# Performance work log

Hardware: AMD Instinct MI355X
Metric: run time of the kernel (lower is better)

## Reference

```python
import jax, jax.numpy as jnp
import numpy as np

DIM = 1024
N_HEADS = 16
HEAD_DIM = DIM // N_HEADS  # 64
THETA = 10000.0
B, S = 4, 1024


def _rope_full_dim(x):
    """RoPE applied over the FULL last dim (head_dim == model dim), matching the
    original module which builds RotaryEmbeddings(head_dim=args.dim) and applies
    it to [B, S, dim] before splitting into heads. Positions start at 0."""
    Bx, Sx, D = x.shape
    freq = 1.0 / (THETA ** (jnp.arange(0, D, 2, dtype=jnp.float32) / D))  # [D/2]
    ang = jnp.arange(Sx, dtype=jnp.float32)[:, None] * freq[None, :]      # [S, D/2]
    cos, sin = jnp.cos(ang), jnp.sin(ang)
    xp = x.astype(jnp.float32).reshape(Bx, Sx, D // 2, 2)
    x0, x1 = xp[..., 0], xp[..., 1]
    rot = jnp.stack([x0 * cos - x1 * sin, x0 * sin + x1 * cos], axis=-1)
    return rot.reshape(Bx, Sx, D).astype(x.dtype)


def setup_inputs() -> dict:
    key = jax.random.key(0)
    ks = jax.random.split(key, 5)
    scale = 1.0 / np.sqrt(DIM)
    x = jax.random.normal(ks[0], (B, S, DIM), dtype=jnp.float32)
    Wq = jax.random.normal(ks[1], (DIM, DIM), dtype=jnp.float32) * scale
    Wk = jax.random.normal(ks[2], (DIM, DIM), dtype=jnp.float32) * scale
    Wv = jax.random.normal(ks[3], (DIM, DIM), dtype=jnp.float32) * scale
    Wo = jax.random.normal(ks[4], (DIM, DIM), dtype=jnp.float32) * scale
    bo = jnp.zeros((DIM,), dtype=jnp.float32)
    return {"x": x, "Wq": Wq, "Wk": Wk, "Wv": Wv, "Wo": Wo, "bo": bo, "start_pos": 0}


def reference(x, Wq, Wk, Wv, Wo, bo, start_pos):
    # start_pos == 0: the zero-initialized KV cache write+read is an identity
    # (keys == xk, values == xv over [:, :S]); n_rep == 1 so repeat_kv is a no-op.
    # NOTE: the original applies NO causal mask.
    Bx, Sx, _ = x.shape
    xq = _rope_full_dim(x @ Wq.T)  # [B, S, DIM] (weights stored torch-style [out,in])
    xk = _rope_full_dim(x @ Wk.T)
    xv = x @ Wv.T
    q = xq.reshape(Bx, Sx, N_HEADS, HEAD_DIM).transpose(0, 2, 1, 3)  # [B,H,S,D]
    k = xk.reshape(Bx, Sx, N_HEADS, HEAD_DIM).transpose(0, 2, 1, 3)
    v = xv.reshape(Bx, Sx, N_HEADS, HEAD_DIM).transpose(0, 2, 1, 3)
    scores = jnp.einsum("bhqd,bhkd->bhqk", q, k) / np.float32(np.sqrt(HEAD_DIM))
    attn = jax.nn.softmax(scores.astype(jnp.float32), axis=-1).astype(q.dtype)
    out = jnp.einsum("bhqk,bhkd->bhqd", attn, v)          # [B,H,S,D]
    out = out.transpose(0, 2, 1, 3).reshape(Bx, Sx, DIM)  # [B,S,DIM]
    return out @ Wo.T + bo
```

## Files before the change

kernel.cpp:

```cpp
#include <hip/hip_runtime.h>
#include <cstdint>
#include <cstddef>

typedef _Float16 f16;
typedef __attribute__((ext_vector_type(8))) _Float16 h8v;
typedef __attribute__((ext_vector_type(4))) _Float16 h4v;
typedef __attribute__((ext_vector_type(4))) float f4v;

#define DIM 1024
#define SEQ 1024
#define NH 16
#define HD 64

__device__ __forceinline__ void gld16(const void* g, void* l) {
  __builtin_amdgcn_global_load_lds(
      (const __attribute__((address_space(1))) void*)g,
      (__attribute__((address_space(3))) void*)l, 16, 0, 0);
}

__device__ __forceinline__ f4v mfma16(h8v a, h8v b, f4v c) {
  return __builtin_amdgcn_mfma_f32_16x16x32_f16(a, b, c, 0, 0, 0);
}
__device__ __forceinline__ f4v mfma16k16(h4v a, h4v b, f4v c) {
  return __builtin_amdgcn_mfma_f32_16x16x16f16(a, b, c, 0, 0, 0);
}

__device__ __forceinline__ void cvt_store4(f16* dst, float4 v) {
  *(h4v*)dst = (h4v){(f16)v.x, (f16)v.y, (f16)v.z, (f16)v.w};
}

__global__ __launch_bounds__(256) void convert_kernel(
    const float* __restrict__ x,  const float* __restrict__ Wq,
    const float* __restrict__ Wk, const float* __restrict__ Wv,
    const float* __restrict__ Wo,
    f16* __restrict__ xh, f16* __restrict__ wqkv, f16* __restrict__ woh)
{
  int i = blockIdx.x * 256 + threadIdx.x;
  cvt_store4(xh + 4 * (size_t)i, ((const float4*)x)[i]);
  if (i < DIM * DIM / 4) {
    cvt_store4(wqkv + 4 * (size_t)i,               ((const float4*)Wq)[i]);
    cvt_store4(wqkv + DIM * DIM + 4 * (size_t)i,   ((const float4*)Wk)[i]);
    cvt_store4(wqkv + 2 * DIM * DIM + 4 * (size_t)i, ((const float4*)Wv)[i]);
    cvt_store4(woh + 4 * (size_t)i,                ((const float4*)Wo)[i]);
  }
}

__global__ __launch_bounds__(256) void qkv_gemm(
    const f16* __restrict__ A, const f16* __restrict__ W,
    f16* __restrict__ Qh, f16* __restrict__ Kh, f16* __restrict__ Vt)
{
  __shared__ f16 lA[128 * 32];
  __shared__ f16 lB[128 * 32];
  const int m0 = blockIdx.x * 128;
  const int n0 = blockIdx.y * 128;
  const int tid = threadIdx.x;
  const int w = tid >> 6, lane = tid & 63, quad = lane >> 4, l16 = lane & 15;
  const int wm = (w >> 1) * 64, wn = (w & 1) * 64;

  const int c0 = tid, c1 = 256 + tid;
  const int r0 = c0 >> 2, kc0 = (c0 & 3) ^ ((r0 >> 1) & 3);
  const int r1 = c1 >> 2, kc1 = (c1 & 3) ^ ((r1 >> 1) & 3);
  const f16* gA0 = A + (size_t)(m0 + r0) * DIM + kc0 * 8;
  const f16* gA1 = A + (size_t)(m0 + r1) * DIM + kc1 * 8;
  const f16* gB0 = W + (size_t)(n0 + r0) * DIM + kc0 * 8;
  const f16* gB1 = W + (size_t)(n0 + r1) * DIM + kc1 * 8;
  f16* lA0 = &lA[(c0 & ~63) * 8];
  f16* lA1 = &lA[(c1 & ~63) * 8];
  f16* lB0 = &lB[(c0 & ~63) * 8];
  f16* lB1 = &lB[(c1 & ~63) * 8];

  int pA[4], pB[4];
#pragma unroll
  for (int t = 0; t < 4; ++t) {
    int r = wm + t * 16 + l16;
    pA[t] = r * 4 + (quad ^ ((r >> 1) & 3));
    int rn = wn + t * 16 + l16;
    pB[t] = rn * 4 + (quad ^ ((rn >> 1) & 3));
  }

  f4v acc[4][4] = {};
  for (int kt = 0; kt < DIM / 32; ++kt) {
    const int ko = kt * 32;
    gld16(gA0 + ko, lA0);
    gld16(gA1 + ko, lA1);
    gld16(gB0 + ko, lB0);
    gld16(gB1 + ko, lB1);
    __syncthreads();
    h8v af[4], bf[4];
#pragma unroll
    for (int t = 0; t < 4; ++t) af[t] = *(const h8v*)&lA[pA[t] * 8];
#pragma unroll
    for (int t = 0; t < 4; ++t) bf[t] = *(const h8v*)&lB[pB[t] * 8];
#pragma unroll
    for (int i = 0; i < 4; ++i)
#pragma unroll
      for (int j = 0; j < 4; ++j)
        acc[i][j] = mfma16(af[i], bf[j], acc[i][j]);
    __syncthreads();
  }

  if (n0 < 2 * DIM) {
    f16* dst = (n0 < DIM) ? Qh : Kh;
    const float osc = (n0 < DIM) ? 0.18033688f : 1.0f;
#pragma unroll
    for (int i = 0; i < 4; ++i) {
      const int mb = m0 + wm + i * 16 + quad * 4;
#pragma unroll
      for (int j = 0; j < 4; ++j) {
        const int n = n0 + wn + j * 16 + l16;
        const int d = n & (DIM - 1);
        const float fr = exp2f(-0.025952563f * (float)(d >> 1));
        const float sgn = (d & 1) ? 1.0f : -1.0f;
        const int hh = d >> 6, dd = d & 63;
#pragma unroll
        for (int r = 0; r < 4; ++r) {
          const int m = mb + r;
          const int s = m & (SEQ - 1), b = m >> 10;
          const float v = acc[i][j][r];
          const float pt = __shfl_xor(v, 1, 64);
          float sn, cs;
          __sincosf((float)s * fr, &sn, &cs);
          dst[((size_t)(b * NH + hh) * SEQ + s) * HD + dd] =
              (f16)((v * cs + sgn * pt * sn) * osc);
        }
      }
    }
  } else {
#pragma unroll
    for (int i = 0; i < 4; ++i) {
      const int mb = m0 + wm + i * 16 + quad * 4;
      const int s = mb & (SEQ - 1), b = mb >> 10;
#pragma unroll
      for (int j = 0; j < 4; ++j) {
        const int d = (n0 - 2 * DIM) + wn + j * 16 + l16;
        const int hh = d >> 6, dd = d & 63;
        h4v vv = {(f16)acc[i][j][0], (f16)acc[i][j][1],
                  (f16)acc[i][j][2], (f16)acc[i][j][3]};
        *(h4v*)&Vt[((size_t)(b * NH + hh) * HD + dd) * SEQ + s] = vv;
      }
    }
  }
}

__global__ __launch_bounds__(256) void attn_kernel(
    const f16* __restrict__ Q, const f16* __restrict__ K,
    const f16* __restrict__ V, f16* __restrict__ O)
{
  __shared__ f16 LK[2][4096];
  __shared__ f16 LV[2][4096];
  const int tid = threadIdx.x;
  const int w = tid >> 6, lane = tid & 63, quad = lane >> 4, l16 = lane & 15;
  const int bid = blockIdx.x;
  const int qt = bid >> 6, bh = bid & 63;
  const f16* Qb = Q + (size_t)bh * SEQ * HD;
  const f16* Kg = K + (size_t)bh * SEQ * HD;
  const f16* Vg = V + (size_t)bh * HD * SEQ;
  const int q0 = qt * 128 + w * 16;

  const h8v bq0a = *(const h8v*)&Qb[(size_t)(q0 + l16) * HD + quad * 8];
  const h8v bq0b = *(const h8v*)&Qb[(size_t)(q0 + l16) * HD + quad * 8 + 32];
  const h8v bq1a = *(const h8v*)&Qb[(size_t)(q0 + 64 + l16) * HD + quad * 8];
  const h8v bq1b = *(const h8v*)&Qb[(size_t)(q0 + 64 + l16) * HD + quad * 8 + 32];

  const int c0 = tid, c1 = 256 + tid;
  const int r0 = c0 >> 3, kc0 = (c0 & 7) ^ (r0 & 7);
  const int r1 = c1 >> 3, kc1 = (c1 & 7) ^ (r1 & 7);
  const f16* gK0 = Kg + (size_t)r0 * HD + kc0 * 8;
  const f16* gK1 = Kg + (size_t)r1 * HD + kc1 * 8;
  const f16* gV0 = Vg + (size_t)r0 * SEQ + kc0 * 8;
  const f16* gV1 = Vg + (size_t)r1 * SEQ + kc1 * 8;
  const int dk0 = (c0 & ~63) * 8, dk1 = (c1 & ~63) * 8;

  int koff[4][2];
#pragma unroll
  for (int j = 0; j < 4; ++j) {
    int r = j * 16 + l16;
#pragma unroll
    for (int kk = 0; kk < 2; ++kk)
      koff[j][kk] = (r * 8 + ((quad + 4 * kk) ^ (r & 7))) * 8;
  }
  int voff[4];
#pragma unroll
  for (int j = 0; j < 4; ++j) {
    int slot = (j * 2 + (quad >> 1)) ^ (l16 & 7);
    voff[j] = l16 * 64 + slot * 8 + (quad & 1) * 4;
  }

  const h4v vones = {(f16)1.f, (f16)1.f, (f16)1.f, (f16)1.f};
  f4v accL0 = {}, accL1 = {};
  f4v accO0[4] = {}, accO1[4] = {};

#define ATTN_PREF(TT, BUF)                       \
  {                                              \
    const size_t kb = (size_t)(TT) * 64;         \
    gld16(gK0 + kb * HD, &LK[BUF][dk0]);         \
    gld16(gK1 + kb * HD, &LK[BUF][dk1]);         \
    gld16(gV0 + kb, &LV[BUF][dk0]);              \
    gld16(gV1 + kb, &LV[BUF][dk1]);              \
  }

#define ATTN_TILE(BUF)                                                       \
  {                                                                          \
    h8v kf[4][2];                                                            \
    _Pragma("unroll")                                                        \
    for (int j = 0; j < 4; ++j) {                                            \
      kf[j][0] = *(const h8v*)&LK[BUF][koff[j][0]];                          \
      kf[j][1] = *(const h8v*)&LK[BUF][koff[j][1]];                          \
    }                                                                        \
    f4v sc0[4], sc1[4];                                                      \
    _Pragma("unroll")                                                        \
    for (int j = 0; j < 4; ++j) {                                            \
      f4v z0 = {-12.f, -12.f, -12.f, -12.f};          \
      z0 = mfma16(kf[j][0], bq0a, z0);                                       \
      z0 = mfma16(kf[j][1], bq0b, z0);                                       \
      sc0[j] = z0;                                                           \
      f4v z1 = {-12.f, -12.f, -12.f, -12.f};                                 \
      z1 = mfma16(kf[j][0], bq1a, z1);                                       \
      z1 = mfma16(kf[j][1], bq1b, z1);                                       \
      sc1[j] = z1;                                                           \
    }                                                                        \
    h4v pf0[4], pf1[4];                                                      \
    _Pragma("unroll")                                                        \
    for (int j = 0; j < 4; ++j) {                                            \
      pf0[j] = (h4v){(f16)exp2f(sc0[j][0]), (f16)exp2f(sc0[j][1]),           \
                     (f16)exp2f(sc0[j][2]), (f16)exp2f(sc0[j][3])};          \
      pf1[j] = (h4v){(f16)exp2f(sc1[j][0]), (f16)exp2f(sc1[j][1]),           \
                     (f16)exp2f(sc1[j][2]), (f16)exp2f(sc1[j][3])};          \
    }                                                                        \
    h4v ps0 = (pf0[0] + pf0[1]) + (pf0[2] + pf0[3]);                         \
    h4v ps1 = (pf1[0] + pf1[1]) + (pf1[2] + pf1[3]);                         \
    accL0 = mfma16k16(ps0, vones, accL0);                                    \
    accL1 = mfma16k16(ps1, vones, accL1);                                    \
    _Pragma("unroll")                                                        \
    for (int dt = 0; dt < 4; ++dt) {                                         \
      _Pragma("unroll")                                                      \
      for (int j = 0; j < 4; ++j) {                                          \
        const h4v vf = *(const h4v*)&LV[BUF][voff[j] + dt * 1024];           \
        accO0[dt] = mfma16k16(pf0[j], vf, accO0[dt]);                        \
        accO1[dt] = mfma16k16(pf1[j], vf, accO1[dt]);                        \
      }                                                                      \
    }                                                                        \
  }

  ATTN_PREF(0, 0);
  for (int t = 0; t < SEQ / 64; t += 2) {
    __syncthreads();
    ATTN_PREF(t + 1, 1);
    ATTN_TILE(0);
    __syncthreads();
    if (t + 2 < SEQ / 64) ATTN_PREF(t + 2, 0);
    ATTN_TILE(1);
  }
#undef ATTN_PREF
#undef ATTN_TILE

  const int b = bh >> 4, hh = bh & 15;
#pragma unroll
  for (int dt = 0; dt < 4; ++dt) {
    const int d = dt * 16 + l16;
#pragma unroll
    for (int r = 0; r < 4; ++r) {
      const int s0 = q0 + quad * 4 + r;
      O[(size_t)(b * SEQ + s0) * DIM + hh * HD + d] =
          (f16)(accO0[dt][r] / accL0[r]);
      O[(size_t)(b * SEQ + s0 + 64) * DIM + hh * HD + d] =
          (f16)(accO1[dt][r] / accL1[r]);
    }
  }
}

__global__ __launch_bounds__(256) void out_gemm(
    const f16* __restrict__ A, const f16* __restrict__ W,
    const float* __restrict__ bias, float* __restrict__ out)
{
  __shared__ f16 lA[64 * 32];
  __shared__ f16 lB[128 * 32];
  const int m0 = blockIdx.x * 64;
  const int n0 = blockIdx.y * 128;
  const int tid = threadIdx.x;
  const int w = tid >> 6, lane = tid & 63, quad = lane >> 4, l16 = lane & 15;
  const int wm = (w >> 1) * 32, wn = (w & 1) * 64;

  const int c0 = tid, c1 = 256 + tid;
  const int rA = c0 >> 2, kcA = (c0 & 3) ^ ((rA >> 1) & 3);
  const int rB1 = c1 >> 2, kcB1 = (c1 & 3) ^ ((rB1 >> 1) & 3);
  const f16* gA  = A + (size_t)(m0 + rA) * DIM + kcA * 8;
  const f16* gB0 = W + (size_t)(n0 + rA) * DIM + kcA * 8;
  const f16* gB1 = W + (size_t)(n0 + rB1) * DIM + kcB1 * 8;
  f16* lAp  = &lA[(c0 & ~63) * 8];
  f16* lB0p = &lB[(c0 & ~63) * 8];
  f16* lB1p = &lB[(c1 & ~63) * 8];

  int pA_[2], pB_[4];
#pragma unroll
  for (int t = 0; t < 2; ++t) {
    int r = wm + t * 16 + l16;
    pA_[t] = r * 4 + (quad ^ ((r >> 1) & 3));
  }
#pragma unroll
  for (int t = 0; t < 4; ++t) {
    int rn = wn + t * 16 + l16;
    pB_[t] = rn * 4 + (quad ^ ((rn >> 1) & 3));
  }

  f4v acc[2][4] = {};
  for (int kt = 0; kt < DIM / 32; ++kt) {
    const int ko = kt * 32;
    gld16(gA + ko, lAp);
    gld16(gB0 + ko, lB0p);
    gld16(gB1 + ko, lB1p);
    __syncthreads();
    h8v af[2], bf[4];
#pragma unroll
    for (int t = 0; t < 2; ++t) af[t] = *(const h8v*)&lA[pA_[t] * 8];
#pragma unroll
    for (int t = 0; t < 4; ++t) bf[t] = *(const h8v*)&lB[pB_[t] * 8];
#pragma unroll
    for (int i = 0; i < 2; ++i)
#pragma unroll
      for (int j = 0; j < 4; ++j)
        acc[i][j] = mfma16(af[i], bf[j], acc[i][j]);
    __syncthreads();
  }

#pragma unroll
  for (int i = 0; i < 2; ++i) {
#pragma unroll
    for (int j = 0; j < 4; ++j) {
      const int n = n0 + wn + j * 16 + l16;
      const float bv = bias[n];
#pragma unroll
      for (int r = 0; r < 4; ++r) {
        const int m = m0 + wm + i * 16 + quad * 4 + r;
        out[(size_t)m * DIM + n] = acc[i][j][r] + bv;
      }
    }
  }
}

extern "C" void kernel_launch(void* const* d_in, const int* in_sizes, int n_in,
                              void* d_out, int out_size, void* d_ws, size_t ws_size,
                              hipStream_t stream)
{
  (void)in_sizes; (void)n_in; (void)out_size; (void)ws_size;
  const float* x  = (const float*)d_in[0];
  const float* Wq = (const float*)d_in[1];
  const float* Wk = (const float*)d_in[2];
  const float* Wv = (const float*)d_in[3];
  const float* Wo = (const float*)d_in[4];
  const float* bo = (const float*)d_in[5];
  float* out = (float*)d_out;

  char* ws = (char*)d_ws;
  const size_t MB = (size_t)1 << 20;
  f16* xh   = (f16*)(ws);
  f16* wqkv = (f16*)(ws + 8  * MB);
  f16* woh  = (f16*)(ws + 14 * MB);
  f16* Qh   = (f16*)(ws + 16 * MB);
  f16* Kh   = (f16*)(ws + 24 * MB);
  f16* Vt   = (f16*)(ws + 32 * MB);
  f16* Oh   = (f16*)(ws);

  convert_kernel<<<dim3(4096), 256, 0, stream>>>(x, Wq, Wk, Wv, Wo, xh, wqkv, woh);
  qkv_gemm<<<dim3(32, 24), 256, 0, stream>>>(xh, wqkv, Qh, Kh, Vt);
  attn_kernel<<<dim3(512), 256, 0, stream>>>(Qh, Kh, Vt, Oh);
  out_gemm<<<dim3(64, 8), 256, 0, stream>>>(Oh, woh, bo, out);
}
```

Baseline: 173.8 us.

## Use hardware transcendentals, packed f16 converts, and permuted V layout for wider LDS reads

```diff
diff --git a/kernel.cpp b/kernel.cpp
--- a/kernel.cpp
+++ b/kernel.cpp
@@ -5,6 +5,7 @@
 typedef _Float16 f16;
 typedef __attribute__((ext_vector_type(8))) _Float16 h8v;
 typedef __attribute__((ext_vector_type(4))) _Float16 h4v;
+typedef __attribute__((ext_vector_type(2))) _Float16 h2v;
 typedef __attribute__((ext_vector_type(4))) float f4v;
 
 #define DIM 1024
@@ -12,6 +13,17 @@
 #define NH 16
 #define HD 64
 
+#if __has_builtin(__builtin_amdgcn_exp2f)
+#define EXP2(x) __builtin_amdgcn_exp2f(x)
+#else
+#define EXP2(x) exp2f(x)
+#endif
+#if __has_builtin(__builtin_amdgcn_rcpf)
+#define RCP(x) __builtin_amdgcn_rcpf(x)
+#else
+#define RCP(x) (1.0f / (x))
+#endif
+
 __device__ __forceinline__ void gld16(const void* g, void* l) {
   __builtin_amdgcn_global_load_lds(
       (const __attribute__((address_space(1))) void*)g,
@@ -23,6 +35,12 @@
 }
 __device__ __forceinline__ f4v mfma16k16(h4v a, h4v b, f4v c) {
   return __builtin_amdgcn_mfma_f32_16x16x16f16(a, b, c, 0, 0, 0);
+}
+
+__device__ __forceinline__ h4v pk4(float a, float b, float c, float d) {
+  h2v lo = __builtin_bit_cast(h2v, __builtin_amdgcn_cvt_pkrtz(a, b));
+  h2v hi = __builtin_bit_cast(h2v, __builtin_amdgcn_cvt_pkrtz(c, d));
+  return (h4v){lo[0], lo[1], hi[0], hi[1]};
 }
 
 __device__ __forceinline__ void cvt_store4(f16* dst, float4 v) {
@@ -102,16 +120,17 @@
   if (n0 < 2 * DIM) {
     f16* dst = (n0 < DIM) ? Qh : Kh;
     const float osc = (n0 < DIM) ? 0.18033688f : 1.0f;
-#pragma unroll
-    for (int i = 0; i < 4; ++i) {
-      const int mb = m0 + wm + i * 16 + quad * 4;
-#pragma unroll
-      for (int j = 0; j < 4; ++j) {
-        const int n = n0 + wn + j * 16 + l16;
-        const int d = n & (DIM - 1);
-        const float fr = exp2f(-0.025952563f * (float)(d >> 1));
-        const float sgn = (d & 1) ? 1.0f : -1.0f;
-        const int hh = d >> 6, dd = d & 63;
+    const float sgn = (l16 & 1) ? 1.0f : -1.0f;
+#pragma unroll
+    for (int j = 0; j < 4; ++j) {
+      const int n = n0 + wn + j * 16 + l16;
+      const int d = n & (DIM - 1);
+      const float fr = exp2f(-0.025952563f * (float)(d >> 1));
+      const float frr = fr * 0.15915494f;
+      const int hh = d >> 6, dd = d & 63;
+#pragma unroll
+      for (int i = 0; i < 4; ++i) {
+        const int mb = m0 + wm + i * 16 + quad * 4;
 #pragma unroll
         for (int r = 0; r < 4; ++r) {
           const int m = mb + r;
@@ -119,7 +138,15 @@
           const float v = acc[i][j][r];
           const float pt = __shfl_xor(v, 1, 64);
           float sn, cs;
-          __sincosf((float)s * fr, &sn, &cs);
+#if __has_builtin(__builtin_amdgcn_sinf) && __has_builtin(__builtin_amdgcn_cosf)
+          float ar = (float)s * frr;
+          ar -= truncf(ar);
+          sn = __builtin_amdgcn_sinf(ar);
+          cs = __builtin_amdgcn_cosf(ar);
+#else
+          float ang = (float)s * fr;
+          sn = __sinf(ang); cs = __cosf(ang);
+#endif
           dst[((size_t)(b * NH + hh) * SEQ + s) * HD + dd] =
               (f16)((v * cs + sgn * pt * sn) * osc);
         }
@@ -129,14 +156,15 @@
 #pragma unroll
     for (int i = 0; i < 4; ++i) {
       const int mb = m0 + wm + i * 16 + quad * 4;
-      const int s = mb & (SEQ - 1), b = mb >> 10;
+      const int b = mb >> 10;
+      const int sp = ((mb & (SEQ - 1)) & ~63) + quad * 16 + i * 4;
 #pragma unroll
       for (int j = 0; j < 4; ++j) {
         const int d = (n0 - 2 * DIM) + wn + j * 16 + l16;
         const int hh = d >> 6, dd = d & 63;
         h4v vv = {(f16)acc[i][j][0], (f16)acc[i][j][1],
                   (f16)acc[i][j][2], (f16)acc[i][j][3]};
-        *(h4v*)&Vt[((size_t)(b * NH + hh) * HD + dd) * SEQ + s] = vv;
+        *(h4v*)&Vt[((size_t)(b * NH + hh) * HD + dd) * SEQ + sp] = vv;
       }
     }
   }
@@ -179,12 +207,10 @@
     for (int kk = 0; kk < 2; ++kk)
       koff[j][kk] = (r * 8 + ((quad + 4 * kk) ^ (r & 7))) * 8;
   }
-  int voff[4];
-#pragma unroll
-  for (int j = 0; j < 4; ++j) {
-    int slot = (j * 2 + (quad >> 1)) ^ (l16 & 7);
-    voff[j] = l16 * 64 + slot * 8 + (quad & 1) * 4;
-  }
+  int voff2[2];
+#pragma unroll
+  for (int jp = 0; jp < 2; ++jp)
+    voff2[jp] = l16 * 64 + ((quad * 2 + jp) ^ (l16 & 7)) * 8;
 
   const h4v vones = {(f16)1.f, (f16)1.f, (f16)1.f, (f16)1.f};
   f4v accL0 = {}, accL1 = {};
@@ -222,10 +248,10 @@
     h4v pf0[4], pf1[4];                                                      \
     _Pragma("unroll")                                                        \
     for (int j = 0; j < 4; ++j) {                                            \
-      pf0[j] = (h4v){(f16)exp2f(sc0[j][0]), (f16)exp2f(sc0[j][1]),           \
-                     (f16)exp2f(sc0[j][2]), (f16)exp2f(sc0[j][3])};          \
-      pf1[j] = (h4v){(f16)exp2f(sc1[j][0]), (f16)exp2f(sc1[j][1]),           \
-                     (f16)exp2f(sc1[j][2]), (f16)exp2f(sc1[j][3])};          \
+      pf0[j] = pk4(EXP2(sc0[j][0]), EXP2(sc0[j][1]),                         \
+                   EXP2(sc0[j][2]), EXP2(sc0[j][3]));                        \
+      pf1[j] = pk4(EXP2(sc1[j][0]), EXP2(sc1[j][1]),                         \
+                   EXP2(sc1[j][2]), EXP2(sc1[j][3]));                        \
     }                                                                        \
     h4v ps0 = (pf0[0] + pf0[1]) + (pf0[2] + pf0[3]);                         \
     h4v ps1 = (pf1[0] + pf1[1]) + (pf1[2] + pf1[3]);                         \
@@ -234,10 +260,14 @@
     _Pragma("unroll")                                                        \
     for (int dt = 0; dt < 4; ++dt) {                                         \
       _Pragma("unroll")                                                      \
-      for (int j = 0; j < 4; ++j) {                                          \
-        const h4v vf = *(const h4v*)&LV[BUF][voff[j] + dt * 1024];           \
-        accO0[dt] = mfma16k16(pf0[j], vf, accO0[dt]);                        \
-        accO1[dt] = mfma16k16(pf1[j], vf, accO1[dt]);                        \
+      for (int jp = 0; jp < 2; ++jp) {                                       \
+        const h8v vv = *(const h8v*)&LV[BUF][voff2[jp] + dt * 1024];         \
+        const h4v vlo = __builtin_shufflevector(vv, vv, 0, 1, 2, 3);         \
+        const h4v vhi = __builtin_shufflevector(vv, vv, 4, 5, 6, 7);         \
+        accO0[dt] = mfma16k16(pf0[2 * jp], vlo, accO0[dt]);                  \
+        accO1[dt] = mfma16k16(pf1[2 * jp], vlo, accO1[dt]);                  \
+        accO0[dt] = mfma16k16(pf0[2 * jp + 1], vhi, accO0[dt]);              \
+        accO1[dt] = mfma16k16(pf1[2 * jp + 1], vhi, accO1[dt]);              \
       }                                                                      \
     }                                                                        \
   }
@@ -253,6 +283,10 @@
   }
 #undef ATTN_PREF
 #undef ATTN_TILE
+
+  f4v inv0, inv1;
+#pragma unroll
+  for (int r = 0; r < 4; ++r) { inv0[r] = RCP(accL0[r]); inv1[r] = RCP(accL1[r]); }
 
   const int b = bh >> 4, hh = bh & 15;
 #pragma unroll
@@ -262,9 +296,9 @@
     for (int r = 0; r < 4; ++r) {
       const int s0 = q0 + quad * 4 + r;
       O[(size_t)(b * SEQ + s0) * DIM + hh * HD + d] =
-          (f16)(accO0[dt][r] / accL0[r]);
+          (f16)(accO0[dt][r] * inv0[r]);
       O[(size_t)(b * SEQ + s0 + 64) * DIM + hh * HD + d] =
-          (f16)(accO1[dt][r] / accL1[r]);
+          (f16)(accO1[dt][r] * inv1[r]);
     }
   }
 }
```

Result: no change. 173.6 us (-0.1%).
